# Kernel tuning notes

Measured on AMD Instinct MI355X. Metric: run time of the kernel, lower is better.

The kernel has to match this reference:

```python
import jax, jax.numpy as jnp
import numpy as np

N_NODES = 50000


def gcn_conv(x, edge_index, W, b, num_nodes):
    """PyG GCNConv: add self-loops, symmetric norm, gather-scatter aggregate."""
    h = x @ W  # [N, out]
    row = jnp.concatenate([edge_index[0], jnp.arange(num_nodes)])  # sources (+ self loops)
    col = jnp.concatenate([edge_index[1], jnp.arange(num_nodes)])  # targets
    deg = jax.ops.segment_sum(jnp.ones_like(col, dtype=h.dtype), col, num_segments=num_nodes)
    dinv = jnp.where(deg > 0, jax.lax.rsqrt(deg), 0.0)
    norm = dinv[row] * dinv[col]  # [E+N]
    msgs = h[row] * norm[:, None]  # gather + scale
    out = jax.ops.segment_sum(msgs, col, num_segments=num_nodes)  # scatter-add
    return out + b


def setup_inputs() -> dict:
    key = jax.random.key(0)
    ks = jax.random.split(key, 8)
    F_in, H, D = 50, 50, 64
    E_train, Ep, En = 1600000, 200000, 200000
    x = jax.random.normal(ks[0], (N_NODES, F_in), dtype=jnp.float32)
    train_pos_edge_index = jax.random.randint(ks[1], (2, E_train), 0, N_NODES)
    pos_edge_index = jax.random.randint(ks[2], (2, Ep), 0, N_NODES)
    neg_edge_index = jax.random.randint(ks[3], (2, En), 0, N_NODES)
    # Glorot-ish params for the two GCN layers
    W1 = jax.random.normal(ks[4], (F_in, H), dtype=jnp.float32) * (1.0 / np.sqrt(F_in))
    b1 = jnp.zeros((H,), dtype=jnp.float32)
    W2 = jax.random.normal(ks[5], (H, D), dtype=jnp.float32) * (1.0 / np.sqrt(H))
    b2 = jnp.zeros((D,), dtype=jnp.float32)
    return {"x": x, "train_pos_edge_index": train_pos_edge_index,
            "pos_edge_index": pos_edge_index, "neg_edge_index": neg_edge_index,
            "W1": W1, "b1": b1, "W2": W2, "b2": b2}


def reference(x, train_pos_edge_index, pos_edge_index, neg_edge_index, W1, b1, W2, b2):
    # encode: conv1 -> relu -> conv2
    h = gcn_conv(x, train_pos_edge_index, W1, b1, N_NODES)
    h = jax.nn.relu(h)
    z = gcn_conv(h, train_pos_edge_index, W2, b2, N_NODES)  # [N, D]
    # decode: dot product over concatenated pos/neg edge endpoints
    edge_index = jnp.concatenate([pos_edge_index, neg_edge_index], axis=-1)
    logits = jnp.sum(z[edge_index[0]] * z[edge_index[1]], axis=-1)  # [Ep+En]
    return logits
```

## Files before the change

kernel.cpp:

```cpp
#include <hip/hip_runtime.h>
#include <hip/hip_bf16.h>
#include <hip/hip_fp16.h>


constexpr int N_NODES = 50000;
constexpr int NBITS = 6;
constexpr int BNODES = 1 << NBITS;
constexpr int NBUCK = (N_NODES + BNODES - 1) / BNODES;
constexpr int CAP = 2560;
constexpr int CHUNK = 6144;
constexpr int PTHREADS = 512;
constexpr int CTHREADS = 512;
constexpr int NTILE = 8;
constexpr int TROWS = 6250;

union H4 {
    uint2 u;
    __half2 h[2];
};

union H8 {
    uint4 u;
    __half2 h[4];
};

__device__ inline H4 f4_to_h4(float4 v) {
    H4 r;
    r.h[0] = __floats2half2_rn(v.x, v.y);
    r.h[1] = __floats2half2_rn(v.z, v.w);
    return r;
}

__device__ inline uint4 pack8(float4 A, float4 B) {
    H8 r;
    r.h[0] = __floats2half2_rn(A.x, A.y);
    r.h[1] = __floats2half2_rn(A.z, A.w);
    r.h[2] = __floats2half2_rn(B.x, B.y);
    r.h[3] = __floats2half2_rn(B.z, B.w);
    return r.u;
}

__device__ inline void unpack8(uint4 w, int* r) {
    r[0] = (int)(w.x & 0xffffu);  r[1] = (int)(w.x >> 16);
    r[2] = (int)(w.y & 0xffffu);  r[3] = (int)(w.y >> 16);
    r[4] = (int)(w.z & 0xffffu);  r[5] = (int)(w.z >> 16);
    r[6] = (int)(w.w & 0xffffu);  r[7] = (int)(w.w >> 16);
}

__device__ inline void add8(float4& A, float4& B, H8 v) {
    float2 g0 = __half22float2(v.h[0]);
    float2 g1 = __half22float2(v.h[1]);
    float2 g2 = __half22float2(v.h[2]);
    float2 g3 = __half22float2(v.h[3]);
    A.x += g0.x; A.y += g0.y; A.z += g1.x; A.w += g1.y;
    B.x += g2.x; B.y += g2.y; B.z += g3.x; B.w += g3.y;
}

__device__ inline void fma8(float4& A, float4& B, H8 v, float m) {
    float2 g0 = __half22float2(v.h[0]);
    float2 g1 = __half22float2(v.h[1]);
    float2 g2 = __half22float2(v.h[2]);
    float2 g3 = __half22float2(v.h[3]);
    A.x = fmaf(m, g0.x, A.x); A.y = fmaf(m, g0.y, A.y);
    A.z = fmaf(m, g1.x, A.z); A.w = fmaf(m, g1.y, A.w);
    B.x = fmaf(m, g2.x, B.x); B.y = fmaf(m, g2.y, B.y);
    B.z = fmaf(m, g3.x, B.z); B.w = fmaf(m, g3.y, B.w);
}

__device__ inline float hdot2(unsigned ua, unsigned ub) {
    __half2 ha = *(__half2*)&ua;
    __half2 hb = *(__half2*)&ub;
    float2 fa = __half22float2(ha);
    float2 fb = __half22float2(hb);
    return fa.x * fb.x + fa.y * fb.y;
}

__global__ __launch_bounds__(PTHREADS) void partition_kernel(const int4* __restrict__ row4,
                                                             const int4* __restrict__ col4, int E,
                                                             int* __restrict__ cursor,
                                                             unsigned* __restrict__ bEdges) {
    __shared__ unsigned ed[CHUNK];
    __shared__ int cnt[NBUCK];
    __shared__ int base[NBUCK];
    int t = threadIdx.x;
    int e0 = blockIdx.x * CHUNK;
    int n = min(CHUNK, E - e0);
    int n4 = n >> 2;
    for (int i = t; i < NBUCK; i += PTHREADS) cnt[i] = 0;
    __syncthreads();
    const int4* r4 = row4 + (e0 >> 2);
    const int4* c4 = col4 + (e0 >> 2);
    for (int i = t; i < n4; i += PTHREADS) {
        int4 r = r4[i];
        int4 c = c4[i];
        ed[i * 4 + 0] = ((unsigned)r.x << 16) | (unsigned)c.x;
        ed[i * 4 + 1] = ((unsigned)r.y << 16) | (unsigned)c.y;
        ed[i * 4 + 2] = ((unsigned)r.z << 16) | (unsigned)c.z;
        ed[i * 4 + 3] = ((unsigned)r.w << 16) | (unsigned)c.w;
        atomicAdd(&cnt[c.x >> NBITS], 1);
        atomicAdd(&cnt[c.y >> NBITS], 1);
        atomicAdd(&cnt[c.z >> NBITS], 1);
        atomicAdd(&cnt[c.w >> NBITS], 1);
    }
    __syncthreads();
    for (int i = t; i < NBUCK; i += PTHREADS) base[i] = cnt[i] ? atomicAdd(&cursor[i], cnt[i]) : 0;
    __syncthreads();
    for (int i = t; i < NBUCK; i += PTHREADS) cnt[i] = 0;
    __syncthreads();
    for (int i = t; i < n; i += PTHREADS) {
        unsigned p = ed[i];
        int bk = (int)(p & 0xffffu) >> NBITS;
        int pos = base[bk] + atomicAdd(&cnt[bk], 1);
        if (pos < CAP) bEdges[(size_t)bk * CAP + pos] = p;
    }
}

__global__ __launch_bounds__(CTHREADS) void bucket_csr_mm_kernel(const int* __restrict__ cursor,
                                                                 const unsigned* __restrict__ bEdges,
                                                                 const float* __restrict__ x,
                                                                 const float* __restrict__ W1,
                                                                 unsigned short* __restrict__ srcIdx,
                                                                 unsigned* __restrict__ rowmeta,
                                                                 float* __restrict__ dinv,
                                                                 uint2* __restrict__ Hs, int N) {
    __shared__ alignas(16) unsigned ed[CAP];
    __shared__ alignas(16) unsigned short srcL[CAP];
    __shared__ unsigned char tick[CAP];
    __shared__ int tdeg[BNODES * NTILE];
    __shared__ int toff[BNODES * NTILE];
    __shared__ int totPad;
    __shared__ float dinvL[BNODES];
    __shared__ float4 Ws4[50 * 16];
    __shared__ float xs[BNODES][51];
    int b = blockIdx.x;
    int tx = threadIdx.x;
    int cnt = min(cursor[b], CAP);
    for (int i = tx; i < BNODES * NTILE; i += CTHREADS) tdeg[i] = 0;
    {
        uint4* z4 = (uint4*)srcL;
        uint4 z = make_uint4(0u, 0u, 0u, 0u);
        for (int i = tx; i < (CAP >> 3); i += CTHREADS) z4[i] = z;
    }
    __syncthreads();
    const uint4* s4 = (const uint4*)(bEdges + (size_t)b * CAP);
    int cnt4 = cnt >> 2;
    for (int i = tx; i < cnt4; i += CTHREADS) {
        uint4 w = s4[i];
        ((uint4*)ed)[i] = w;
        unsigned pp[4] = {w.x, w.y, w.z, w.w};
#pragma unroll
        for (int u = 0; u < 4; ++u) {
            unsigned p = pp[u];
            int l = (int)(p & (BNODES - 1));
            int tl = (int)(p >> 16) / TROWS;
            tick[i * 4 + u] = (unsigned char)atomicAdd(&tdeg[l * NTILE + tl], 1);
        }
    }
    for (int i = cnt4 * 4 + tx; i < cnt; i += CTHREADS) {
        unsigned p = bEdges[(size_t)b * CAP + i];
        ed[i] = p;
        int l = (int)(p & (BNODES - 1));
        int tl = (int)(p >> 16) / TROWS;
        tick[i] = (unsigned char)atomicAdd(&tdeg[l * NTILE + tl], 1);
    }
    for (int i = tx; i < 50 * 64; i += CTHREADS) {
        int k = i >> 6;
        int c = i & 63;
        ((float*)Ws4)[i] = (c < 50) ? W1[k * 50 + c] : 0.f;
    }
    for (int i = tx; i < BNODES * 50; i += CTHREADS) {
        int l = i / 50;
        int k = i - l * 50;
        int node = b * BNODES + l;
        xs[l][k] = (node < N) ? x[(size_t)node * 50 + k] : 0.f;
    }
    __syncthreads();
    if (tx < BNODES) {
        int sd[NTILE];
        int d = 0;
#pragma unroll
        for (int u = 0; u < NTILE; ++u) {
            sd[u] = tdeg[tx * NTILE + u];
            d += sd[u];
        }
        int dpad = (d + 7) & ~7;
        int s = dpad;
#pragma unroll
        for (int off = 1; off < BNODES; off <<= 1) {
            int o = __shfl_up(s, off, 64);
            if (tx >= off) s += o;
        }
        int ex = s - dpad;
        int run = ex;
#pragma unroll
        for (int u = 0; u < NTILE; ++u) {
            toff[tx * NTILE + u] = run;
            run += sd[u];
        }
        if (tx == 63) totPad = min(s, CAP);
        float dvv = rsqrtf((float)d + 1.0f);
        dinvL[tx] = dvv;
        int node = b * BNODES + tx;
        if (node < N) {
            unsigned st = (unsigned)(b * CAP + ex);
            rowmeta[node] = (st << 7) | (unsigned)d;
            dinv[node] = dvv;
        }
    }
    __syncthreads();
    for (int i = tx; i < cnt; i += CTHREADS) {
        unsigned p = ed[i];
        int l = (int)(p & (BNODES - 1));
        int tl = (int)(p >> 16) / TROWS;
        int pos = toff[l * NTILE + tl] + (int)tick[i];
        if (pos < CAP) srcL[pos] = (unsigned short)(p >> 16);
    }
    __syncthreads();
    int tot = totPad;
    {
        const uint4* sl4 = (const uint4*)srcL;
        uint4* si4 = (uint4*)(srcIdx + (size_t)b * CAP);
        for (int i = tx; i < (tot >> 3); i += CTHREADS) si4[i] = sl4[i];
    }
    int q = tx & 15;
    int g = tx >> 4;
#pragma unroll
    for (int rep = 0; rep < 2; ++rep) {
        int l = g + rep * 32;
        float4 acc = make_float4(0.f, 0.f, 0.f, 0.f);
#pragma unroll
        for (int k = 0; k < 50; ++k) {
            float xv = xs[l][k];
            float4 w = Ws4[k * 16 + q];
            acc.x = fmaf(xv, w.x, acc.x);
            acc.y = fmaf(xv, w.y, acc.y);
            acc.z = fmaf(xv, w.z, acc.z);
            acc.w = fmaf(xv, w.w, acc.w);
        }
        float dv = dinvL[l];
        acc.x *= dv;
        acc.y *= dv;
        acc.z *= dv;
        acc.w *= dv;
        int node = b * BNODES + l;
        if (node < N) Hs[(size_t)node * 16 + q] = f4_to_h4(acc).u;
    }
}

__device__ inline void gather_sum8(const unsigned short* __restrict__ srcIdx,
                                   const uint4* __restrict__ hs, int node, int q,
                                   unsigned meta, float4& A, float4& B) {
    int start = (int)(meta >> 7);
    int d = (int)(meta & 127u);
    int end = start + d;
    H8 t;
    t.u = hs[(size_t)node * 8 + q];
    {
        float2 g0 = __half22float2(t.h[0]);
        float2 g1 = __half22float2(t.h[1]);
        float2 g2 = __half22float2(t.h[2]);
        float2 g3 = __half22float2(t.h[3]);
        A = make_float4(g0.x, g0.y, g1.x, g1.y);
        B = make_float4(g2.x, g2.y, g3.x, g3.y);
    }
    if (d == 0) return;
    int j = start;
    uint4 w = *(const uint4*)(srcIdx + j);
    while (j + 8 <= end) {
        uint4 wc = w;
        if (j + 8 < end) w = *(const uint4*)(srcIdx + j + 8);
        int r[8];
        unpack8(wc, r);
#pragma unroll
        for (int u = 0; u < 8; ++u) {
            H8 hv;
            hv.u = hs[(size_t)r[u] * 8 + q];
            add8(A, B, hv);
        }
        j += 8;
    }
    if (j < end) {
        int r[8];
        unpack8(w, r);
#pragma unroll
        for (int u = 0; u < 8; ++u) {
            float m = (j + u < end) ? 1.f : 0.f;
            H8 hv;
            hv.u = hs[(size_t)r[u] * 8 + q];
            fma8(A, B, hv, m);
        }
    }
}

template <int BC>
__global__ __launch_bounds__(256) void agg_mm_kernel(const unsigned* __restrict__ rowmeta,
                                                     const unsigned short* __restrict__ srcIdx,
                                                     const uint4* __restrict__ hs,
                                                     const float* __restrict__ dinv,
                                                     const float* __restrict__ b1,
                                                     const float* __restrict__ W2,
                                                     uint4* __restrict__ out, int N) {
    __shared__ float4 Ws4[50 * 16];
    __shared__ float h1s[32][68];
    for (int i = threadIdx.x; i < 50 * 64; i += 256) ((float*)Ws4)[i] = W2[i];
    int tid = blockIdx.x * blockDim.x + threadIdx.x;
    int node = tid >> 3;
    int q = tid & 7;
    int g = threadIdx.x >> 3;
    int nodeC = min(node, N - 1);
    float4 A = make_float4(0.f, 0.f, 0.f, 0.f), B = A;
    if (q < 7) gather_sum8(srcIdx, hs, nodeC, q, rowmeta[nodeC], A, B);
    float dv = dinv[nodeC];
    int f = q * 8;
    float hv[8] = {A.x, A.y, A.z, A.w, B.x, B.y, B.z, B.w};
#pragma unroll
    for (int u = 0; u < 8; ++u) {
        float bb = (f + u < BC) ? b1[f + u] : 0.f;
        h1s[g][f + u] = fmaxf(dv * hv[u] + bb, 0.f);
    }
    __syncthreads();
    float4 aA = make_float4(0.f, 0.f, 0.f, 0.f), aB = aA;
#pragma unroll
    for (int k = 0; k < 50; ++k) {
        float xv = h1s[g][k];
        float4 wA = Ws4[k * 16 + 2 * q];
        float4 wB = Ws4[k * 16 + 2 * q + 1];
        aA.x = fmaf(xv, wA.x, aA.x);
        aA.y = fmaf(xv, wA.y, aA.y);
        aA.z = fmaf(xv, wA.z, aA.z);
        aA.w = fmaf(xv, wA.w, aA.w);
        aB.x = fmaf(xv, wB.x, aB.x);
        aB.y = fmaf(xv, wB.y, aB.y);
        aB.z = fmaf(xv, wB.z, aB.z);
        aB.w = fmaf(xv, wB.w, aB.w);
    }
    aA.x *= dv; aA.y *= dv; aA.z *= dv; aA.w *= dv;
    aB.x *= dv; aB.y *= dv; aB.z *= dv; aB.w *= dv;
    if (node < N) out[(size_t)node * 8 + q] = pack8(aA, aB);
}

template <int BC>
__global__ __launch_bounds__(256) void agg_kernel(const unsigned* __restrict__ rowmeta,
                                                  const unsigned short* __restrict__ srcIdx,
                                                  const uint4* __restrict__ hs,
                                                  const float* __restrict__ dinv,
                                                  const float* __restrict__ b,
                                                  uint4* __restrict__ out, int N) {
    int tid = blockIdx.x * blockDim.x + threadIdx.x;
    int node = tid >> 3;
    int q = tid & 7;
    if (node >= N) return;
    float4 A, B;
    gather_sum8(srcIdx, hs, node, q, rowmeta[node], A, B);
    float dv = dinv[node];
    int f = q * 8;
    float hv[8] = {A.x, A.y, A.z, A.w, B.x, B.y, B.z, B.w};
    float o[8];
#pragma unroll
    for (int u = 0; u < 8; ++u) o[u] = dv * hv[u] + (f + u < BC ? b[f + u] : 0.f);
    out[(size_t)node * 8 + q] =
        pack8(make_float4(o[0], o[1], o[2], o[3]), make_float4(o[4], o[5], o[6], o[7]));
}

__global__ __launch_bounds__(256) void decode_kernel(const int* __restrict__ pos,
                                                     const int* __restrict__ neg, int Ep, int En,
                                                     const uint4* __restrict__ z4,
                                                     float* __restrict__ logits) {
    int tid = blockIdx.x * blockDim.x + threadIdx.x;
    int e = tid >> 3;
    int q = tid & 7;
    int Etot = Ep + En;
    if (e >= Etot) return;
    int a, bn;
    if (e < Ep) {
        a = pos[e];
        bn = pos[Ep + e];
    } else {
        int t = e - Ep;
        a = neg[t];
        bn = neg[En + t];
    }
    uint4 ua = z4[(size_t)a * 8 + q];
    uint4 ub = z4[(size_t)bn * 8 + q];
    float v = hdot2(ua.x, ub.x) + hdot2(ua.y, ub.y) + hdot2(ua.z, ub.z) + hdot2(ua.w, ub.w);
    v += __shfl_xor(v, 1, 64);
    v += __shfl_xor(v, 2, 64);
    v += __shfl_xor(v, 4, 64);
    if (q == 0) logits[e] = v;
}

extern "C" void kernel_launch(void* const* d_in, const int* in_sizes, int n_in,
                              void* d_out, int out_size, void* d_ws, size_t ws_size,
                              hipStream_t stream) {
    const float* x = (const float*)d_in[0];
    const int* train = (const int*)d_in[1];
    const int* pos = (const int*)d_in[2];
    const int* neg = (const int*)d_in[3];
    const float* W1 = (const float*)d_in[4];
    const float* b1 = (const float*)d_in[5];
    const float* W2 = (const float*)d_in[6];
    const float* b2 = (const float*)d_in[7];
    float* logits = (float*)d_out;

    const int FIN = 50;
    const int N = in_sizes[0] / FIN;
    const int E = in_sizes[1] / 2;
    const int Ep = in_sizes[2] / 2;
    const int En = in_sizes[3] / 2;

    const int* t_row = train;
    const int* t_col = train + E;

    float* dinv = (float*)d_ws;
    __half* buf0 = (__half*)(dinv + N);
    __half* buf1 = buf0 + (size_t)N * 64;
    unsigned* rowmeta = (unsigned*)(buf1 + (size_t)N * 64);
    int* cursor = (int*)(rowmeta + N);
    uintptr_t sp = (uintptr_t)(cursor + NBUCK);
    sp = (sp + 15) & ~(uintptr_t)15;
    unsigned short* srcIdx = (unsigned short*)sp;
    uintptr_t bp = (uintptr_t)(srcIdx + (size_t)NBUCK * CAP);
    bp = (bp + 15) & ~(uintptr_t)15;
    unsigned* bEdges = (unsigned*)bp;

    hipMemsetAsync(cursor, 0, (size_t)NBUCK * sizeof(int), stream);

    partition_kernel<<<(E + CHUNK - 1) / CHUNK, PTHREADS, 0, stream>>>((const int4*)t_row,
                                                                       (const int4*)t_col, E,
                                                                       cursor, bEdges);
    bucket_csr_mm_kernel<<<NBUCK, CTHREADS, 0, stream>>>(cursor, bEdges, x, W1, srcIdx, rowmeta,
                                                         dinv, (uint2*)buf0, N);

    const int AGB = (N * 8 + 255) / 256;

    agg_mm_kernel<50><<<AGB, 256, 0, stream>>>(rowmeta, srcIdx, (const uint4*)buf0, dinv, b1, W2,
                                               (uint4*)buf1, N);
    agg_kernel<64><<<AGB, 256, 0, stream>>>(rowmeta, srcIdx, (const uint4*)buf1, dinv, b2,
                                            (uint4*)buf0, N);
    decode_kernel<<<((Ep + En) * 8 + 255) / 256, 256, 0, stream>>>(pos, neg, Ep, En,
                                                                   (const uint4*)buf0, logits);
}
```

Before: 204.0 us.

## Locally counting-sort edges by bucket in LDS before global scatter

The partition kernel now records each edge's per-bucket ticket from the shared-memory atomic and computes exclusive bucket offsets with a wave-level prefix scan. Edges are scattered in LDS into bucket-sorted order, then written out in that order so consecutive threads store to contiguous bucket slots. The aim is more coalesced global writes and no second round of shared atomics. The cost is a re-read of row/col from global memory, an extra byte-per-edge ticket array, and a serial per-thread scan over bucket segments.

```diff
diff --git a/kernel.cpp b/kernel.cpp
--- a/kernel.cpp
+++ b/kernel.cpp
@@ -79,8 +79,10 @@
                                                              const int4* __restrict__ col4, int E,
                                                              int* __restrict__ cursor,
                                                              unsigned* __restrict__ bEdges) {
-    __shared__ unsigned ed[CHUNK];
+    __shared__ unsigned ed2[CHUNK];
+    __shared__ unsigned char tick[CHUNK];
     __shared__ int cnt[NBUCK];
+    __shared__ int loff[NBUCK];
     __shared__ int base[NBUCK];
     int t = threadIdx.x;
     int e0 = blockIdx.x * CHUNK;
@@ -91,26 +93,51 @@
     const int4* r4 = row4 + (e0 >> 2);
     const int4* c4 = col4 + (e0 >> 2);
     for (int i = t; i < n4; i += PTHREADS) {
+        int4 c = c4[i];
+        tick[i * 4 + 0] = (unsigned char)atomicAdd(&cnt[c.x >> NBITS], 1);
+        tick[i * 4 + 1] = (unsigned char)atomicAdd(&cnt[c.y >> NBITS], 1);
+        tick[i * 4 + 2] = (unsigned char)atomicAdd(&cnt[c.z >> NBITS], 1);
+        tick[i * 4 + 3] = (unsigned char)atomicAdd(&cnt[c.w >> NBITS], 1);
+    }
+    __syncthreads();
+    if (t < 64) {
+        constexpr int SEG = (NBUCK + 63) / 64;
+        int lo = t * SEG;
+        int hi = min(lo + SEG, NBUCK);
+        int s = 0;
+        for (int i = lo; i < hi; ++i) {
+            loff[i] = s;
+            s += cnt[i];
+        }
+        int tot = s;
+        int ex = tot;
+#pragma unroll
+        for (int off = 1; off < 64; off <<= 1) {
+            int o = __shfl_up(ex, off, 64);
+            if (t >= off) ex += o;
+        }
+        ex -= tot;
+        for (int i = lo; i < hi; ++i) loff[i] += ex;
+    }
+    __syncthreads();
+    for (int i = t; i < NBUCK; i += PTHREADS) base[i] = cnt[i] ? atomicAdd(&cursor[i], cnt[i]) : 0;
+    for (int i = t; i < n4; i += PTHREADS) {
         int4 r = r4[i];
         int4 c = c4[i];
-        ed[i * 4 + 0] = ((unsigned)r.x << 16) | (unsigned)c.x;
-        ed[i * 4 + 1] = ((unsigned)r.y << 16) | (unsigned)c.y;
-        ed[i * 4 + 2] = ((unsigned)r.z << 16) | (unsigned)c.z;
-        ed[i * 4 + 3] = ((unsigned)r.w << 16) | (unsigned)c.w;
-        atomicAdd(&cnt[c.x >> NBITS], 1);
-        atomicAdd(&cnt[c.y >> NBITS], 1);
-        atomicAdd(&cnt[c.z >> NBITS], 1);
-        atomicAdd(&cnt[c.w >> NBITS], 1);
-    }
-    __syncthreads();
-    for (int i = t; i < NBUCK; i += PTHREADS) base[i] = cnt[i] ? atomicAdd(&cursor[i], cnt[i]) : 0;
-    __syncthreads();
-    for (int i = t; i < NBUCK; i += PTHREADS) cnt[i] = 0;
-    __syncthreads();
-    for (int i = t; i < n; i += PTHREADS) {
-        unsigned p = ed[i];
+        unsigned p0 = ((unsigned)r.x << 16) | (unsigned)c.x;
+        unsigned p1 = ((unsigned)r.y << 16) | (unsigned)c.y;
+        unsigned p2 = ((unsigned)r.z << 16) | (unsigned)c.z;
+        unsigned p3 = ((unsigned)r.w << 16) | (unsigned)c.w;
+        ed2[loff[c.x >> NBITS] + (int)tick[i * 4 + 0]] = p0;
+        ed2[loff[c.y >> NBITS] + (int)tick[i * 4 + 1]] = p1;
+        ed2[loff[c.z >> NBITS] + (int)tick[i * 4 + 2]] = p2;
+        ed2[loff[c.w >> NBITS] + (int)tick[i * 4 + 3]] = p3;
+    }
+    __syncthreads();
+    for (int s = t; s < n; s += PTHREADS) {
+        unsigned p = ed2[s];
         int bk = (int)(p & 0xffffu) >> NBITS;
-        int pos = base[bk] + atomicAdd(&cnt[bk], 1);
+        int pos = base[bk] + (s - loff[bk]);
         if (pos < CAP) bEdges[(size_t)bk * CAP + pos] = p;
     }
 }
```

New measurement: 197.5 us. 1.03x faster.
